# Optimization experiments

Measured on AMD Instinct MI355X. Metric: run time of the kernel, lower is better.

The kernel has to match this reference:

```python
import jax, jax.numpy as jnp
import numpy as np

# ---- static configuration (matches init_kwargs / input_specs) ----
B, DIM, H, W = 2, 32, 512, 512
FOLD, P, HDIM, NCLS, CV = 8, 2, 96, 16, 96
S = P * P                      # superpixels per tile
h, w = H // FOLD, W // FOLD    # 64, 64 tile size
N = h * w                      # pixels per tile

# ---- static SSN neighbor tables (init label map -> 9 candidate spixels) ----
_lab = np.repeat(np.repeat(np.arange(S).reshape(P, P), h // P, 0), w // P, 1).reshape(-1)
_sy, _sx = _lab // P, _lab % P
_dy = np.repeat(np.array([-1, 0, 1]), 3)[:, None]
_dx = np.tile(np.array([-1, 0, 1]), 3)[:, None]
_ny, _nx = _sy[None] + _dy, _sx[None] + _dx
_valid = (_ny >= 0) & (_ny < P) & (_nx >= 0) & (_nx < P)
NBR = jnp.asarray(np.where(_valid, _ny * P + _nx, 0), dtype=jnp.int32)  # [9,N]
VALID = jnp.asarray(_valid)                                             # [9,N]

def _conv1x1(x, Wk, bk):
    return jnp.einsum('oc,bchw->bohw', Wk, x) + bk[None, :, None, None]

def _tiles(t):  # 'b c (f1 h) (f2 w) -> (b f1 f2) c h w'
    Bq, C = t.shape[:2]
    return t.reshape(Bq, C, FOLD, h, FOLD, w).transpose(0, 2, 4, 1, 3, 5).reshape(Bq * FOLD * FOLD, C, h, w)

def _pool(t):  # adaptive avg pool (h,w)->(P,P); returns [b,C,S]
    b, C = t.shape[:2]
    return t.reshape(b, C, P, h // P, P, w // P).mean((3, 5)).reshape(b, C, S)

def _affinity(Fp, cen):
    # Fp [b,Ctot,N], cen [b,Ctot,S]; squared-euclid dist pixel->9 neighbor spixels,
    # sparse softmax over the 9 candidates, then scatter to dense [b,S,N] affinity.
    d = (Fp * Fp).sum(1)[:, None, :] + (cen * cen).sum(1)[:, :, None] \
        - 2.0 * jnp.einsum('bcn,bcs->bsn', Fp, cen)          # [b,S,N]
    b = Fp.shape[0]
    idx = jnp.broadcast_to(NBR[None], (b, 9, N))
    d9 = jnp.where(VALID[None], jnp.take_along_axis(d, idx, axis=1), 1e16)
    aff = jax.nn.softmax(-d9, axis=1)                        # [b,9,N]
    bi = jnp.arange(b)[:, None, None]
    ni = jnp.arange(N)[None, None, :]
    return jnp.zeros((b, S, N), Fp.dtype).at[bi, idx, ni].add(jnp.where(VALID[None], aff, 0.0))

def setup_inputs():
    k = jax.random.split(jax.random.key(0), 6)
    return {
        'x': jax.random.normal(k[0], (B, DIM, H, W), jnp.float32),
        'feat': jax.random.normal(k[1], (B, CV, H, W), jnp.float32),
        'sdf_data': jax.random.normal(k[2], (B, DIM - 1, H, W), jnp.float32),
        'Wf': 0.1 * jax.random.normal(k[3], (HDIM, DIM), jnp.float32),
        'bf': jnp.zeros((HDIM,), jnp.float32),
        'Wsdf': 0.1 * jax.random.normal(k[4], (HDIM, DIM - 1), jnp.float32),
        'bsdf': jnp.zeros((HDIM,), jnp.float32),
        'gt': jax.random.randint(k[5], (B, H, W), 0, NCLS, jnp.int32),
    }

def _cluster(x, feat, sdf_data, Wf, bf, Wsdf, bsdf):
    hsi = _conv1x1(x, Wf, bf)
    sdf = _conv1x1(sdf_data, Wsdf, bsdf)
    pf = _tiles(feat).reshape(-1, CV, N)      # per-tile pixel (value) features
    df = _tiles(hsi).reshape(-1, HDIM, N)     # deep features
    sf = _tiles(sdf).reshape(-1, HDIM, N)     # sdf features
    b = pf.shape[0]
    cen_pf = _pool(pf.reshape(b, CV, h, w))
    cen_df = _pool(df.reshape(b, HDIM, h, w))
    cen_sf = _pool(sf.reshape(b, HDIM, h, w))
    value_centers = cen_pf.transpose(0, 2, 1)                # [b,S,C]
    Fall = jnp.concatenate([pf, df, sf], 1)
    # SSN iter 0: soft affinity, update pixel-feature centroids
    A0 = _affinity(Fall, jnp.concatenate([cen_pf, cen_df, cen_sf], 1))
    cen_pf = jnp.einsum('bsn,bcn->bcs', A0, pf) / (A0.sum(-1)[:, None, :] + 1e-16)
    # SSN iter 1 (last): final dense affinity; torch computes this under no_grad
    sim = jax.lax.stop_gradient(_affinity(Fall, jnp.concatenate([cen_pf, cen_df, cen_sf], 1)))
    mask = jax.nn.one_hot(jnp.argmax(sim, 1), S, axis=1, dtype=sim.dtype)   # hard argmax mask [b,S,N]
    sim = sim * mask
    out = (jnp.einsum('bsn,bnc->bsc', sim, pf.transpose(0, 2, 1)) + value_centers) \
          / (sim.sum(-1, keepdims=True) + 1.0)
    center_feat = out.reshape(B, FOLD * FOLD * S, CV)
    mask5 = mask.reshape(B, FOLD * FOLD, S, h, w)
    return center_feat, mask5

def _gen_labels(gt, mask5):
    T = FOLD * FOLD
    coef = jnp.arange(S, dtype=mask5.dtype).reshape(1, 1, S, 1, 1)
    small = (mask5 * coef).sum(2) + jnp.arange(0, T * S, S, dtype=mask5.dtype).reshape(1, T, 1, 1)
    spix_map = small.reshape(B, FOLD, FOLD, h, w).transpose(0, 1, 3, 2, 4).reshape(B, H, W)
    gt_r = gt.reshape(B, FOLD, h, FOLD, w).transpose(0, 1, 3, 2, 4).reshape(B, T, h, w) + 1
    gt_filt = (gt_r[:, :, None].astype(mask5.dtype) * mask5).reshape(B, T, S, N).astype(jnp.int32)
    count = jax.nn.one_hot(gt_filt, NCLS + 1, dtype=jnp.float32).sum(3)   # [B,T,S,NCLS+1]
    labels = count[..., 1:].transpose(0, 3, 1, 2).reshape(B, NCLS, T * S)
    return labels, spix_map

def reference(x, feat, sdf_data, Wf, bf, Wsdf, bsdf, gt):
    center_feat, mask5 = _cluster(x, feat, sdf_data, Wf, bf, Wsdf, bsdf)
    labels, spix_map = _gen_labels(gt, jax.lax.stop_gradient(mask5))
    return center_feat, labels, spix_map
```

## Files before the change

kernel.cpp:

```cpp
#include <hip/hip_runtime.h>
#include <hip/hip_bf16.h>


#define OFF_POOLX   0
#define OFF_POOLS   16384
#define OFF_CENPF0  32256
#define OFF_UDF     81408
#define OFF_USF     97792
#define OFF_GCONST  113664
#define OFF_NORM0   114176
#define OFF_NUM1    114688
#define OFF_DEN1    163840
#define OFF_CENPF1  164352
#define OFF_NORM1   213504
#define OFF_OUTNUM  214016
#define OFF_OUTDEN  263168
#define OFF_LABELS  263680
#define OFF_G       271872

#define OUT_CF 0
#define OUT_LB 49152
#define OUT_SP 57344

__device__ __forceinline__ float bf2f(unsigned short u) {
  return __uint_as_float(((unsigned)u) << 16);
}
__device__ __forceinline__ unsigned short f2bf(float f) {
  return (unsigned short)(__float_as_uint(f) >> 16);
}

__global__ __launch_bounds__(256) void k_pool(const float* __restrict__ x,
    const float* __restrict__ feat, const float* __restrict__ sdf,
    float* __restrict__ ws) {
  int tile = blockIdx.y, ch = blockIdx.x, tid = threadIdx.x;
  const float* src; int c, C; float* dst;
  if (ch < 32)      { src = x;    C = 32; c = ch;      dst = ws + OFF_POOLX  + (tile*32 + c)*4; }
  else if (ch < 63) { src = sdf;  C = 31; c = ch - 32; dst = ws + OFF_POOLS  + (tile*31 + c)*4; }
  else              { src = feat; C = 96; c = ch - 63; dst = ws + OFF_CENPF0 + (tile*96 + c)*4; }
  int b = tile >> 6, tl = tile & 63, f1 = tl >> 3, f2 = tl & 7;
  const float* base = src + ((size_t)(b*C + c)*512 + f1*64)*512 + f2*64;
  float acc0 = 0.f, acc1 = 0.f;
  #pragma unroll
  for (int i = 0; i < 4; ++i) {
    int vi = i*256 + tid;
    int y = vi >> 4, xv = vi & 15;
    const float4* p = reinterpret_cast<const float4*>(base + (size_t)y*512 + xv*4);
    float4 v = *p;
    float s4 = v.x + v.y + v.z + v.w;
    if (i < 2) acc0 += s4; else acc1 += s4;
  }
  acc0 += __shfl_xor(acc0, 1, 64); acc0 += __shfl_xor(acc0, 2, 64); acc0 += __shfl_xor(acc0, 4, 64);
  acc1 += __shfl_xor(acc1, 1, 64); acc1 += __shfl_xor(acc1, 2, 64); acc1 += __shfl_xor(acc1, 4, 64);
  __shared__ float part[64];
  int lane = tid & 63, wave = tid >> 6;
  if ((lane & 7) == 0) {
    int g = lane >> 3, qx = g & 1, gj = g >> 1;
    part[qx*16       + wave*4 + gj] = acc0;
    part[(2 + qx)*16 + wave*4 + gj] = acc1;
  }
  __syncthreads();
  if (tid < 64) {
    float v = part[tid];
    v += __shfl_xor(v, 1, 64); v += __shfl_xor(v, 2, 64);
    v += __shfl_xor(v, 4, 64); v += __shfl_xor(v, 8, 64);
    if ((tid & 15) == 0) dst[tid >> 4] = v * (1.f/1024.f);
  }
}

__global__ __launch_bounds__(384) void k_centers(const float* __restrict__ Wf,
    const float* __restrict__ bfv, const float* __restrict__ Wsdf,
    const float* __restrict__ bsdf, float* __restrict__ ws) {
  int tile = blockIdx.x, tid = threadIdx.x;
  __shared__ float px[128];
  __shared__ float ps[124];
  __shared__ float cdf[384];
  __shared__ float csf[384];
  __shared__ float redg[4], redn[4];
  if (tid < 128) px[tid] = ws[OFF_POOLX + tile*128 + tid];
  if (tid < 124) ps[tid] = ws[OFF_POOLS + tile*124 + tid];
  if (tid < 4) { redg[tid] = 0.f; redn[tid] = 0.f; }
  __syncthreads();
  int c = tid % 96, s = tid / 96;
  float bc = bfv[c];
  float a = bc;
  for (int k = 0; k < 32; ++k) a += Wf[c*32 + k] * px[k*4 + s];
  cdf[c*4 + s] = a;
  float bs = bsdf[c];
  float a2 = bs;
  for (int k = 0; k < 31; ++k) a2 += Wsdf[c*31 + k] * ps[k*4 + s];
  csf[c*4 + s] = a2;
  atomicAdd(&redg[s], 2.f*(bc*a + bs*a2) - (a*a + a2*a2));
  float cp = ws[OFF_CENPF0 + tile*384 + c*4 + s];
  atomicAdd(&redn[s], cp*cp);
  __syncthreads();
  if (tid < 128) {
    int s2 = tid >> 5, k = tid & 31;
    float u = 0.f;
    for (int c2 = 0; c2 < 96; ++c2) u += Wf[c2*32 + k] * cdf[c2*4 + s2];
    ws[OFF_UDF + tile*128 + tid] = u;
  } else if (tid < 252) {
    int t2 = tid - 128, s2 = t2 / 31, k = t2 % 31;
    float u = 0.f;
    for (int c2 = 0; c2 < 96; ++c2) u += Wsdf[c2*31 + k] * csf[c2*4 + s2];
    ws[OFF_USF + tile*124 + t2] = u;
  }
  if (tid < 4) { ws[OFF_GCONST + tile*4 + tid] = redg[tid]; ws[OFF_NORM0 + tile*4 + tid] = redn[tid]; }
}

__global__ __launch_bounds__(256) void k_pass2(const float* __restrict__ x,
    const float* __restrict__ feat, const float* __restrict__ sdf,
    float* __restrict__ ws) {
  int wg = blockIdx.x, tile = wg >> 2, seg = wg & 3, tid = threadIdx.x;
  int b = tile >> 6, tl = tile & 63, f1 = tl >> 3, f2 = tl & 7;
  __shared__ float s_cpf0[384];
  __shared__ float s_udf[128];
  __shared__ float s_usf[124];
  __shared__ float s_gc[4], s_n0[4];
  __shared__ float s_A0[4][257];
  __shared__ unsigned short s_pf[256][98];
  for (int i = tid; i < 384; i += 256) s_cpf0[i] = ws[OFF_CENPF0 + tile*384 + i];
  if (tid < 128) s_udf[tid] = ws[OFF_UDF + tile*128 + tid];
  if (tid < 124) s_usf[tid] = ws[OFF_USF + tile*124 + tid];
  if (tid < 4) { s_gc[tid] = ws[OFF_GCONST + tile*4 + tid]; s_n0[tid] = ws[OFF_NORM0 + tile*4 + tid]; }
  __syncthreads();
  int cA = tid % 96, sA = tid / 96;
  int cB = (tid + 256) % 96, sB = (tid + 256) / 96;
  float accA = 0.f, accB = 0.f;
  float dden[4] = {0.f, 0.f, 0.f, 0.f};
  for (int chunk = 0; chunk < 4; ++chunk) {
    int p = seg*1024 + chunk*256 + tid;
    int y = p >> 6, xx = p & 63;
    int go = (f1*64 + y)*512 + f2*64 + xx;
    float d0=0.f,d1=0.f,d2=0.f,d3=0.f;
    for (int k = 0; k < 32; ++k) {
      float v = x[(b*32 + k)*262144 + go];
      d0 += v*s_udf[k]; d1 += v*s_udf[32+k]; d2 += v*s_udf[64+k]; d3 += v*s_udf[96+k];
    }
    for (int k = 0; k < 31; ++k) {
      float v = sdf[(b*31 + k)*262144 + go];
      d0 += v*s_usf[k]; d1 += v*s_usf[31+k]; d2 += v*s_usf[62+k]; d3 += v*s_usf[93+k];
    }
    float g0 = 2.f*d0 + s_gc[0], g1 = 2.f*d1 + s_gc[1];
    float g2 = 2.f*d2 + s_gc[2], g3 = 2.f*d3 + s_gc[3];
    int gbase = OFF_G + (tile << 14) + p;
    ws[gbase] = g0; ws[gbase + 4096] = g1; ws[gbase + 8192] = g2; ws[gbase + 12288] = g3;
    float p0=0.f,p1=0.f,p2=0.f,p3=0.f;
    for (int c = 0; c < 96; ++c) {
      float v = feat[(b*96 + c)*262144 + go];
      s_pf[tid][c] = f2bf(v);
      p0 += v*s_cpf0[c*4+0]; p1 += v*s_cpf0[c*4+1]; p2 += v*s_cpf0[c*4+2]; p3 += v*s_cpf0[c*4+3];
    }
    float sc0 = g0 + 2.f*p0 - s_n0[0];
    float sc1 = g1 + 2.f*p1 - s_n0[1];
    float sc2 = g2 + 2.f*p2 - s_n0[2];
    float sc3 = g3 + 2.f*p3 - s_n0[3];
    float m = fmaxf(fmaxf(sc0, sc1), fmaxf(sc2, sc3));
    float e0 = expf(sc0 - m), e1 = expf(sc1 - m), e2 = expf(sc2 - m), e3 = expf(sc3 - m);
    float inv = 1.f / (e0 + e1 + e2 + e3);
    float a0 = e0*inv, a1 = e1*inv, a2 = e2*inv, a3 = e3*inv;
    s_A0[0][tid] = a0; s_A0[1][tid] = a1; s_A0[2][tid] = a2; s_A0[3][tid] = a3;
    dden[0] += a0; dden[1] += a1; dden[2] += a2; dden[3] += a3;
    __syncthreads();
    if (tid < 128) {
      for (int n = 0; n < 256; ++n) {
        accA += s_A0[sA][n] * bf2f(s_pf[n][cA]);
        accB += s_A0[sB][n] * bf2f(s_pf[n][cB]);
      }
    } else {
      for (int n = 0; n < 256; ++n) accA += s_A0[sA][n] * bf2f(s_pf[n][cA]);
    }
    __syncthreads();
  }
  atomicAdd(&ws[OFF_NUM1 + (tile*96 + cA)*4 + sA], accA);
  if (tid < 128) atomicAdd(&ws[OFF_NUM1 + (tile*96 + cB)*4 + sB], accB);
  for (int m2 = 1; m2 < 64; m2 <<= 1) {
    dden[0] += __shfl_xor(dden[0], m2, 64); dden[1] += __shfl_xor(dden[1], m2, 64);
    dden[2] += __shfl_xor(dden[2], m2, 64); dden[3] += __shfl_xor(dden[3], m2, 64);
  }
  if ((tid & 63) == 0) {
    atomicAdd(&ws[OFF_DEN1 + tile*4 + 0], dden[0]);
    atomicAdd(&ws[OFF_DEN1 + tile*4 + 1], dden[1]);
    atomicAdd(&ws[OFF_DEN1 + tile*4 + 2], dden[2]);
    atomicAdd(&ws[OFF_DEN1 + tile*4 + 3], dden[3]);
  }
}

__global__ __launch_bounds__(384) void k_fin1(float* __restrict__ ws) {
  int tile = blockIdx.x, tid = threadIdx.x;
  __shared__ float red[4];
  if (tid < 4) red[tid] = 0.f;
  __syncthreads();
  int c = tid % 96, s = tid / 96;
  float den = ws[OFF_DEN1 + tile*4 + s];
  float v = ws[OFF_NUM1 + (tile*96 + c)*4 + s] / (den + 1e-16f);
  ws[OFF_CENPF1 + (tile*96 + c)*4 + s] = v;
  atomicAdd(&red[s], v*v);
  __syncthreads();
  if (tid < 4) ws[OFF_NORM1 + tile*4 + tid] = red[tid];
}

__global__ __launch_bounds__(256) void k_pass3(const float* __restrict__ feat,
    const int* __restrict__ gt, float* __restrict__ ws, float* __restrict__ out) {
  int wg = blockIdx.x, tile = wg >> 2, seg = wg & 3, tid = threadIdx.x;
  int b = tile >> 6, tl = tile & 63, f1 = tl >> 3, f2 = tl & 7;
  __shared__ float s_cpf1[384];
  __shared__ float s_n1[4];
  __shared__ float s_W[4][257];
  __shared__ unsigned short s_pf[256][98];
  __shared__ float s_hist[64];
  for (int i = tid; i < 384; i += 256) s_cpf1[i] = ws[OFF_CENPF1 + tile*384 + i];
  if (tid < 4) s_n1[tid] = ws[OFF_NORM1 + tile*4 + tid];
  if (tid < 64) s_hist[tid] = 0.f;
  __syncthreads();
  int cA = tid % 96, sA = tid / 96;
  int cB = (tid + 256) % 96, sB = (tid + 256) / 96;
  float accA = 0.f, accB = 0.f;
  float oden[4] = {0.f, 0.f, 0.f, 0.f};
  for (int chunk = 0; chunk < 4; ++chunk) {
    int p = seg*1024 + chunk*256 + tid;
    int y = p >> 6, xx = p & 63;
    int go = (f1*64 + y)*512 + f2*64 + xx;
    int gbase = OFF_G + (tile << 14) + p;
    float g0 = ws[gbase], g1 = ws[gbase + 4096], g2 = ws[gbase + 8192], g3 = ws[gbase + 12288];
    float p0=0.f,p1=0.f,p2=0.f,p3=0.f;
    for (int c = 0; c < 96; ++c) {
      float v = feat[(b*96 + c)*262144 + go];
      s_pf[tid][c] = f2bf(v);
      p0 += v*s_cpf1[c*4+0]; p1 += v*s_cpf1[c*4+1]; p2 += v*s_cpf1[c*4+2]; p3 += v*s_cpf1[c*4+3];
    }
    float sc0 = g0 + 2.f*p0 - s_n1[0];
    float sc1 = g1 + 2.f*p1 - s_n1[1];
    float sc2 = g2 + 2.f*p2 - s_n1[2];
    float sc3 = g3 + 2.f*p3 - s_n1[3];
    int ss = 0; float best = sc0;
    if (sc1 > best) { best = sc1; ss = 1; }
    if (sc2 > best) { best = sc2; ss = 2; }
    if (sc3 > best) { best = sc3; ss = 3; }
    float se = expf(sc0-best) + expf(sc1-best) + expf(sc2-best) + expf(sc3-best);
    float sim = 1.f / se;
    s_W[0][tid] = (ss == 0) ? sim : 0.f;
    s_W[1][tid] = (ss == 1) ? sim : 0.f;
    s_W[2][tid] = (ss == 2) ? sim : 0.f;
    s_W[3][tid] = (ss == 3) ? sim : 0.f;
    oden[ss] += sim;
    int gv = gt[b*262144 + go];
    atomicAdd(&s_hist[ss*16 + gv], 1.f);
    out[OUT_SP + b*262144 + go] = (float)(tl*4 + ss);
    __syncthreads();
    if (tid < 128) {
      for (int n = 0; n < 256; ++n) {
        accA += s_W[sA][n] * bf2f(s_pf[n][cA]);
        accB += s_W[sB][n] * bf2f(s_pf[n][cB]);
      }
    } else {
      for (int n = 0; n < 256; ++n) accA += s_W[sA][n] * bf2f(s_pf[n][cA]);
    }
    __syncthreads();
  }
  atomicAdd(&ws[OFF_OUTNUM + (tile*96 + cA)*4 + sA], accA);
  if (tid < 128) atomicAdd(&ws[OFF_OUTNUM + (tile*96 + cB)*4 + sB], accB);
  for (int m2 = 1; m2 < 64; m2 <<= 1) {
    oden[0] += __shfl_xor(oden[0], m2, 64); oden[1] += __shfl_xor(oden[1], m2, 64);
    oden[2] += __shfl_xor(oden[2], m2, 64); oden[3] += __shfl_xor(oden[3], m2, 64);
  }
  if ((tid & 63) == 0) {
    atomicAdd(&ws[OFF_OUTDEN + tile*4 + 0], oden[0]);
    atomicAdd(&ws[OFF_OUTDEN + tile*4 + 1], oden[1]);
    atomicAdd(&ws[OFF_OUTDEN + tile*4 + 2], oden[2]);
    atomicAdd(&ws[OFF_OUTDEN + tile*4 + 3], oden[3]);
  }
  if (tid < 64) atomicAdd(&ws[OFF_LABELS + tile*64 + tid], s_hist[tid]);
}

__global__ __launch_bounds__(384) void k_out(const float* __restrict__ ws,
                                             float* __restrict__ out) {
  int tile = blockIdx.x, tid = threadIdx.x;
  int b = tile >> 6, tl = tile & 63;
  int c = tid % 96, s = tid / 96;
  float od = ws[OFF_OUTDEN + tile*4 + s];
  float v = (ws[OFF_OUTNUM + (tile*96 + c)*4 + s] + ws[OFF_CENPF0 + (tile*96 + c)*4 + s]) / (od + 1.f);
  out[OUT_CF + (size_t)(b*256 + tl*4 + s)*96 + c] = v;
  if (tid < 64) {
    int s2 = tid >> 4, cls = tid & 15;
    float cnt = ws[OFF_LABELS + tile*64 + tid];
    out[OUT_LB + (b*16 + cls)*256 + tl*4 + s2] = cnt;
  }
}

extern "C" void kernel_launch(void* const* d_in, const int* in_sizes, int n_in,
                              void* d_out, int out_size, void* d_ws, size_t ws_size,
                              hipStream_t stream) {
  const float* x    = (const float*)d_in[0];
  const float* feat = (const float*)d_in[1];
  const float* sdf  = (const float*)d_in[2];
  const float* Wf   = (const float*)d_in[3];
  const float* bfv  = (const float*)d_in[4];
  const float* Wsdf = (const float*)d_in[5];
  const float* bsdf = (const float*)d_in[6];
  const int* gt = (const int*)d_in[7];
  float* ws = (float*)d_ws;
  float* out = (float*)d_out;

  hipMemsetAsync(ws + OFF_NUM1, 0,
                 (size_t)(OFF_LABELS + 128*64 - OFF_NUM1) * sizeof(float), stream);

  k_pool   <<<dim3(159, 128), 256, 0, stream>>>(x, feat, sdf, ws);
  k_centers<<<128, 384, 0, stream>>>(Wf, bfv, Wsdf, bsdf, ws);
  k_pass2  <<<512, 256, 0, stream>>>(x, feat, sdf, ws);
  k_fin1   <<<128, 384, 0, stream>>>(ws);
  k_pass3  <<<512, 256, 0, stream>>>(feat, gt, ws, out);
  k_out    <<<128, 384, 0, stream>>>(ws, out);
}
```

Baseline: 545.4 us.

## Use bf16 MFMA for center accumulation and pool full-row strips

Replaces the scalar LDS dot-product loops in pass2 and pass3, which accumulate weighted feature sums per superpixel, with 16x16x32 bf16 MFMA instructions. It stores the pixel features and affinities transposed in LDS with padded rows so each lane can load 8-element fragments. The affinity weights are now rounded to bf16 (features already were), and the superpixel dimension is zero-padded to 16, which wastes part of each MFMA. Separately, the pooling kernel now reads full 512-wide row strips per block, covering eight tiles per block instead of one 64x64 tile, to get longer contiguous reads and fewer blocks.

```diff
diff --git a/kernel.cpp b/kernel.cpp
--- a/kernel.cpp
+++ b/kernel.cpp
@@ -22,6 +22,9 @@
 #define OUT_LB 49152
 #define OUT_SP 57344
 
+typedef float f32x4 __attribute__((ext_vector_type(4)));
+typedef short bf16x8 __attribute__((ext_vector_type(8)));
+
 __device__ __forceinline__ float bf2f(unsigned short u) {
   return __uint_as_float(((unsigned)u) << 16);
 }
@@ -32,38 +35,41 @@
 __global__ __launch_bounds__(256) void k_pool(const float* __restrict__ x,
     const float* __restrict__ feat, const float* __restrict__ sdf,
     float* __restrict__ ws) {
-  int tile = blockIdx.y, ch = blockIdx.x, tid = threadIdx.x;
-  const float* src; int c, C; float* dst;
-  if (ch < 32)      { src = x;    C = 32; c = ch;      dst = ws + OFF_POOLX  + (tile*32 + c)*4; }
-  else if (ch < 63) { src = sdf;  C = 31; c = ch - 32; dst = ws + OFF_POOLS  + (tile*31 + c)*4; }
-  else              { src = feat; C = 96; c = ch - 63; dst = ws + OFF_CENPF0 + (tile*96 + c)*4; }
-  int b = tile >> 6, tl = tile & 63, f1 = tl >> 3, f2 = tl & 7;
-  const float* base = src + ((size_t)(b*C + c)*512 + f1*64)*512 + f2*64;
+  int plane = blockIdx.x, f1 = blockIdx.y, tid = threadIdx.x;
+  int b = plane / 159, ch = plane % 159;
+  const float* src; int c, C, cls;
+  if (ch < 32)      { src = x;    C = 32; c = ch;      cls = 0; }
+  else if (ch < 63) { src = sdf;  C = 31; c = ch - 32; cls = 1; }
+  else              { src = feat; C = 96; c = ch - 63; cls = 2; }
+  const float* base = src + ((size_t)(b*C + c)*512 + f1*64)*512;
+  int half = tid >> 7, col4 = tid & 127;
   float acc0 = 0.f, acc1 = 0.f;
-  #pragma unroll
-  for (int i = 0; i < 4; ++i) {
-    int vi = i*256 + tid;
-    int y = vi >> 4, xv = vi & 15;
-    const float4* p = reinterpret_cast<const float4*>(base + (size_t)y*512 + xv*4);
-    float4 v = *p;
+  #pragma unroll 4
+  for (int i = 0; i < 32; ++i) {
+    int y = 2*i + half;
+    float4 v = *reinterpret_cast<const float4*>(base + (size_t)y*512 + col4*4);
     float s4 = v.x + v.y + v.z + v.w;
-    if (i < 2) acc0 += s4; else acc1 += s4;
+    if (i < 16) acc0 += s4; else acc1 += s4;
   }
   acc0 += __shfl_xor(acc0, 1, 64); acc0 += __shfl_xor(acc0, 2, 64); acc0 += __shfl_xor(acc0, 4, 64);
   acc1 += __shfl_xor(acc1, 1, 64); acc1 += __shfl_xor(acc1, 2, 64); acc1 += __shfl_xor(acc1, 4, 64);
-  __shared__ float part[64];
-  int lane = tid & 63, wave = tid >> 6;
+  __shared__ float part[32][2];
+  int lane = tid & 63;
   if ((lane & 7) == 0) {
-    int g = lane >> 3, qx = g & 1, gj = g >> 1;
-    part[qx*16       + wave*4 + gj] = acc0;
-    part[(2 + qx)*16 + wave*4 + gj] = acc1;
-  }
-  __syncthreads();
-  if (tid < 64) {
-    float v = part[tid];
-    v += __shfl_xor(v, 1, 64); v += __shfl_xor(v, 2, 64);
-    v += __shfl_xor(v, 4, 64); v += __shfl_xor(v, 8, 64);
-    if ((tid & 15) == 0) dst[tid >> 4] = v * (1.f/1024.f);
+    int f2 = col4 >> 4, qx = (col4 >> 3) & 1;
+    part[(f2*2 + qx)*2 + 0][half] = acc0;
+    part[(f2*2 + qx)*2 + 1][half] = acc1;
+  }
+  __syncthreads();
+  if (tid < 32) {
+    float v = (part[tid][0] + part[tid][1]) * (1.f/1024.f);
+    int f2 = tid >> 2, qx = (tid >> 1) & 1, qy = tid & 1;
+    int tile = b*64 + f1*8 + f2, s = qy*2 + qx;
+    float* dst;
+    if (cls == 0)      dst = ws + OFF_POOLX  + (tile*32 + c)*4;
+    else if (cls == 1) dst = ws + OFF_POOLS  + (tile*31 + c)*4;
+    else               dst = ws + OFF_CENPF0 + (tile*96 + c)*4;
+    dst[s] = v;
   }
 }
 
@@ -116,16 +122,18 @@
   __shared__ float s_udf[128];
   __shared__ float s_usf[124];
   __shared__ float s_gc[4], s_n0[4];
-  __shared__ float s_A0[4][257];
-  __shared__ unsigned short s_pf[256][98];
+  __shared__ __align__(16) unsigned short s_pfT[96][264];
+  __shared__ __align__(16) unsigned short s_aT[16][264];
   for (int i = tid; i < 384; i += 256) s_cpf0[i] = ws[OFF_CENPF0 + tile*384 + i];
   if (tid < 128) s_udf[tid] = ws[OFF_UDF + tile*128 + tid];
   if (tid < 124) s_usf[tid] = ws[OFF_USF + tile*124 + tid];
   if (tid < 4) { s_gc[tid] = ws[OFF_GCONST + tile*4 + tid]; s_n0[tid] = ws[OFF_NORM0 + tile*4 + tid]; }
-  __syncthreads();
-  int cA = tid % 96, sA = tid / 96;
-  int cB = (tid + 256) % 96, sB = (tid + 256) / 96;
-  float accA = 0.f, accB = 0.f;
+  for (int i = tid; i < 16*264; i += 256) (&s_aT[0][0])[i] = 0;
+  __syncthreads();
+  int lane = tid & 63, wave = tid >> 6;
+  int mrow = lane & 15, quad = lane >> 4;
+  f32x4 zero4 = {0.f, 0.f, 0.f, 0.f};
+  f32x4 accC[6] = {zero4, zero4, zero4, zero4, zero4, zero4};
   float dden[4] = {0.f, 0.f, 0.f, 0.f};
   for (int chunk = 0; chunk < 4; ++chunk) {
     int p = seg*1024 + chunk*256 + tid;
@@ -145,10 +153,10 @@
     int gbase = OFF_G + (tile << 14) + p;
     ws[gbase] = g0; ws[gbase + 4096] = g1; ws[gbase + 8192] = g2; ws[gbase + 12288] = g3;
     float p0=0.f,p1=0.f,p2=0.f,p3=0.f;
-    for (int c = 0; c < 96; ++c) {
-      float v = feat[(b*96 + c)*262144 + go];
-      s_pf[tid][c] = f2bf(v);
-      p0 += v*s_cpf0[c*4+0]; p1 += v*s_cpf0[c*4+1]; p2 += v*s_cpf0[c*4+2]; p3 += v*s_cpf0[c*4+3];
+    for (int cc = 0; cc < 96; ++cc) {
+      float v = feat[(b*96 + cc)*262144 + go];
+      s_pfT[cc][tid] = f2bf(v);
+      p0 += v*s_cpf0[cc*4+0]; p1 += v*s_cpf0[cc*4+1]; p2 += v*s_cpf0[cc*4+2]; p3 += v*s_cpf0[cc*4+3];
     }
     float sc0 = g0 + 2.f*p0 - s_n0[0];
     float sc1 = g1 + 2.f*p1 - s_n0[1];
@@ -158,26 +166,36 @@
     float e0 = expf(sc0 - m), e1 = expf(sc1 - m), e2 = expf(sc2 - m), e3 = expf(sc3 - m);
     float inv = 1.f / (e0 + e1 + e2 + e3);
     float a0 = e0*inv, a1 = e1*inv, a2 = e2*inv, a3 = e3*inv;
-    s_A0[0][tid] = a0; s_A0[1][tid] = a1; s_A0[2][tid] = a2; s_A0[3][tid] = a3;
+    s_aT[0][tid] = f2bf(a0); s_aT[1][tid] = f2bf(a1);
+    s_aT[2][tid] = f2bf(a2); s_aT[3][tid] = f2bf(a3);
     dden[0] += a0; dden[1] += a1; dden[2] += a2; dden[3] += a3;
     __syncthreads();
-    if (tid < 128) {
-      for (int n = 0; n < 256; ++n) {
-        accA += s_A0[sA][n] * bf2f(s_pf[n][cA]);
-        accB += s_A0[sB][n] * bf2f(s_pf[n][cB]);
+    #pragma unroll
+    for (int kk = 0; kk < 2; ++kk) {
+      int k0 = (wave*2 + kk)*32 + quad*8;
+      bf16x8 bfrag = *reinterpret_cast<const bf16x8*>(&s_aT[mrow][k0]);
+      #pragma unroll
+      for (int mt = 0; mt < 6; ++mt) {
+        bf16x8 afrag = *reinterpret_cast<const bf16x8*>(&s_pfT[mt*16 + mrow][k0]);
+        accC[mt] = __builtin_amdgcn_mfma_f32_16x16x32_bf16(afrag, bfrag, accC[mt], 0, 0, 0);
       }
-    } else {
-      for (int n = 0; n < 256; ++n) accA += s_A0[sA][n] * bf2f(s_pf[n][cA]);
     }
     __syncthreads();
   }
-  atomicAdd(&ws[OFF_NUM1 + (tile*96 + cA)*4 + sA], accA);
-  if (tid < 128) atomicAdd(&ws[OFF_NUM1 + (tile*96 + cB)*4 + sB], accB);
+  if (mrow < 4) {
+    #pragma unroll
+    for (int mt = 0; mt < 6; ++mt)
+      #pragma unroll
+      for (int r = 0; r < 4; ++r) {
+        int c = mt*16 + quad*4 + r;
+        atomicAdd(&ws[OFF_NUM1 + (tile*96 + c)*4 + mrow], accC[mt][r]);
+      }
+  }
   for (int m2 = 1; m2 < 64; m2 <<= 1) {
     dden[0] += __shfl_xor(dden[0], m2, 64); dden[1] += __shfl_xor(dden[1], m2, 64);
     dden[2] += __shfl_xor(dden[2], m2, 64); dden[3] += __shfl_xor(dden[3], m2, 64);
   }
-  if ((tid & 63) == 0) {
+  if (lane == 0) {
     atomicAdd(&ws[OFF_DEN1 + tile*4 + 0], dden[0]);
     atomicAdd(&ws[OFF_DEN1 + tile*4 + 1], dden[1]);
     atomicAdd(&ws[OFF_DEN1 + tile*4 + 2], dden[2]);
@@ -205,16 +223,18 @@
   int b = tile >> 6, tl = tile & 63, f1 = tl >> 3, f2 = tl & 7;
   __shared__ float s_cpf1[384];
   __shared__ float s_n1[4];
-  __shared__ float s_W[4][257];
-  __shared__ unsigned short s_pf[256][98];
+  __shared__ __align__(16) unsigned short s_pfT[96][264];
+  __shared__ __align__(16) unsigned short s_aT[16][264];
   __shared__ float s_hist[64];
   for (int i = tid; i < 384; i += 256) s_cpf1[i] = ws[OFF_CENPF1 + tile*384 + i];
   if (tid < 4) s_n1[tid] = ws[OFF_NORM1 + tile*4 + tid];
   if (tid < 64) s_hist[tid] = 0.f;
-  __syncthreads();
-  int cA = tid % 96, sA = tid / 96;
-  int cB = (tid + 256) % 96, sB = (tid + 256) / 96;
-  float accA = 0.f, accB = 0.f;
+  for (int i = tid; i < 16*264; i += 256) (&s_aT[0][0])[i] = 0;
+  __syncthreads();
+  int lane = tid & 63, wave = tid >> 6;
+  int mrow = lane & 15, quad = lane >> 4;
+  f32x4 zero4 = {0.f, 0.f, 0.f, 0.f};
+  f32x4 accC[6] = {zero4, zero4, zero4, zero4, zero4, zero4};
   float oden[4] = {0.f, 0.f, 0.f, 0.f};
   for (int chunk = 0; chunk < 4; ++chunk) {
     int p = seg*1024 + chunk*256 + tid;
@@ -223,10 +243,10 @@
     int gbase = OFF_G + (tile << 14) + p;
     float g0 = ws[gbase], g1 = ws[gbase + 4096], g2 = ws[gbase + 8192], g3 = ws[gbase + 12288];
     float p0=0.f,p1=0.f,p2=0.f,p3=0.f;
-    for (int c = 0; c < 96; ++c) {
-      float v = feat[(b*96 + c)*262144 + go];
-      s_pf[tid][c] = f2bf(v);
-      p0 += v*s_cpf1[c*4+0]; p1 += v*s_cpf1[c*4+1]; p2 += v*s_cpf1[c*4+2]; p3 += v*s_cpf1[c*4+3];
+    for (int cc = 0; cc < 96; ++cc) {
+      float v = feat[(b*96 + cc)*262144 + go];
+      s_pfT[cc][tid] = f2bf(v);
+      p0 += v*s_cpf1[cc*4+0]; p1 += v*s_cpf1[cc*4+1]; p2 += v*s_cpf1[cc*4+2]; p3 += v*s_cpf1[cc*4+3];
     }
     float sc0 = g0 + 2.f*p0 - s_n1[0];
     float sc1 = g1 + 2.f*p1 - s_n1[1];
@@ -238,32 +258,42 @@
     if (sc3 > best) { best = sc3; ss = 3; }
     float se = expf(sc0-best) + expf(sc1-best) + expf(sc2-best) + expf(sc3-best);
     float sim = 1.f / se;
-    s_W[0][tid] = (ss == 0) ? sim : 0.f;
-    s_W[1][tid] = (ss == 1) ? sim : 0.f;
-    s_W[2][tid] = (ss == 2) ? sim : 0.f;
-    s_W[3][tid] = (ss == 3) ? sim : 0.f;
+    unsigned short sb = f2bf(sim);
+    s_aT[0][tid] = (ss == 0) ? sb : (unsigned short)0;
+    s_aT[1][tid] = (ss == 1) ? sb : (unsigned short)0;
+    s_aT[2][tid] = (ss == 2) ? sb : (unsigned short)0;
+    s_aT[3][tid] = (ss == 3) ? sb : (unsigned short)0;
     oden[ss] += sim;
     int gv = gt[b*262144 + go];
     atomicAdd(&s_hist[ss*16 + gv], 1.f);
     out[OUT_SP + b*262144 + go] = (float)(tl*4 + ss);
     __syncthreads();
-    if (tid < 128) {
-      for (int n = 0; n < 256; ++n) {
-        accA += s_W[sA][n] * bf2f(s_pf[n][cA]);
-        accB += s_W[sB][n] * bf2f(s_pf[n][cB]);
+    #pragma unroll
+    for (int kk = 0; kk < 2; ++kk) {
+      int k0 = (wave*2 + kk)*32 + quad*8;
+      bf16x8 bfrag = *reinterpret_cast<const bf16x8*>(&s_aT[mrow][k0]);
+      #pragma unroll
+      for (int mt = 0; mt < 6; ++mt) {
+        bf16x8 afrag = *reinterpret_cast<const bf16x8*>(&s_pfT[mt*16 + mrow][k0]);
+        accC[mt] = __builtin_amdgcn_mfma_f32_16x16x32_bf16(afrag, bfrag, accC[mt], 0, 0, 0);
       }
-    } else {
-      for (int n = 0; n < 256; ++n) accA += s_W[sA][n] * bf2f(s_pf[n][cA]);
     }
     __syncthreads();
   }
-  atomicAdd(&ws[OFF_OUTNUM + (tile*96 + cA)*4 + sA], accA);
-  if (tid < 128) atomicAdd(&ws[OFF_OUTNUM + (tile*96 + cB)*4 + sB], accB);
+  if (mrow < 4) {
+    #pragma unroll
+    for (int mt = 0; mt < 6; ++mt)
+      #pragma unroll
+      for (int r = 0; r < 4; ++r) {
+        int c = mt*16 + quad*4 + r;
+        atomicAdd(&ws[OFF_OUTNUM + (tile*96 + c)*4 + mrow], accC[mt][r]);
+      }
+  }
   for (int m2 = 1; m2 < 64; m2 <<= 1) {
     oden[0] += __shfl_xor(oden[0], m2, 64); oden[1] += __shfl_xor(oden[1], m2, 64);
     oden[2] += __shfl_xor(oden[2], m2, 64); oden[3] += __shfl_xor(oden[3], m2, 64);
   }
-  if ((tid & 63) == 0) {
+  if (lane == 0) {
     atomicAdd(&ws[OFF_OUTDEN + tile*4 + 0], oden[0]);
     atomicAdd(&ws[OFF_OUTDEN + tile*4 + 1], oden[1]);
     atomicAdd(&ws[OFF_OUTDEN + tile*4 + 2], oden[2]);
@@ -304,7 +334,7 @@
   hipMemsetAsync(ws + OFF_NUM1, 0,
                  (size_t)(OFF_LABELS + 128*64 - OFF_NUM1) * sizeof(float), stream);
 
-  k_pool   <<<dim3(159, 128), 256, 0, stream>>>(x, feat, sdf, ws);
+  k_pool   <<<dim3(318, 8), 256, 0, stream>>>(x, feat, sdf, ws);
   k_centers<<<128, 384, 0, stream>>>(Wf, bfv, Wsdf, bsdf, ws);
   k_pass2  <<<512, 256, 0, stream>>>(x, feat, sdf, ws);
   k_fin1   <<<128, 384, 0, stream>>>(ws);
```

New measurement: 520.3 us. 1.05x faster.
